# Performance work log

Hardware: AMD Instinct MI355X
Metric: run time of the kernel (lower is better)

Reference implementation:

```python
import jax, jax.numpy as jnp
import numpy as np

N, L, C = 4, 2048, 512
H, D = 8, 64          # head_num, head_channels; H*D == C so proj_in/out are Identity
FF = 4 * C            # GEGLU inner channels = 2048
EPS = 1e-5


def _layernorm(x, g, b):
    m = jnp.mean(x, axis=-1, keepdims=True)
    v = jnp.var(x, axis=-1, keepdims=True)
    return (x - m) * jax.lax.rsqrt(v + EPS) * g + b


def setup_inputs() -> dict:
    key = jax.random.key(0)
    ks = jax.random.split(key, 8)
    s = 0.02
    return {
        "x": jax.random.normal(ks[0], (N, L, C), dtype=jnp.float32),
        "ln0_g": jnp.ones((C,), jnp.float32),
        "ln0_b": jnp.zeros((C,), jnp.float32),
        "Wq": jax.random.normal(ks[1], (C, H * D), jnp.float32) * s,
        "bq": jnp.zeros((H * D,), jnp.float32),
        "Wk": jax.random.normal(ks[2], (C, H * D), jnp.float32) * s,
        "bk": jnp.zeros((H * D,), jnp.float32),
        "Wv": jax.random.normal(ks[3], (C, H * D), jnp.float32) * s,
        "bv": jnp.zeros((H * D,), jnp.float32),
        "ln1_g": jnp.ones((C,), jnp.float32),
        "ln1_b": jnp.zeros((C,), jnp.float32),
        "Wp": jax.random.normal(ks[4], (C, 2 * FF), jnp.float32) * s,
        "bp": jnp.zeros((2 * FF,), jnp.float32),
        "W2": jax.random.normal(ks[5], (FF, C), jnp.float32) * s,
        "b2": jnp.zeros((C,), jnp.float32),
    }


def reference(x, ln0_g, ln0_b, Wq, bq, Wk, bk, Wv, bv, ln1_g, ln1_b, Wp, bp, W2, b2):
    n, l, _ = x.shape
    # ---- self attention (CrossAttn with context = x) ----
    h = _layernorm(x, ln0_g, ln0_b)
    q = (h @ Wq + bq).reshape(n, l, H, D).transpose(0, 2, 1, 3)  # [n,H,l,D]
    k = (h @ Wk + bk).reshape(n, l, H, D).transpose(0, 2, 1, 3)
    v = (h @ Wv + bv).reshape(n, l, H, D).transpose(0, 2, 1, 3)
    scores = jnp.einsum('nhld,nhmd->nhlm', q, k) * (D ** -0.5)   # [n,H,l,l]
    attn = jax.nn.softmax(scores, axis=-1)
    o = jnp.einsum('nhlm,nhmd->nhld', attn, v)
    o = o.transpose(0, 2, 1, 3).reshape(n, l, H * D)
    # inner_channels == in_channels -> output projection is Identity (dropout=0)
    x = x + o
    # ---- feed forward: LayerNorm -> GEGLU -> Linear, residual ----
    h2 = _layernorm(x, ln1_g, ln1_b)
    pg = h2 @ Wp + bp                      # [n,l,2*FF]
    u, g = jnp.split(pg, 2, axis=-1)
    y = u * jax.nn.gelu(g, approximate=False)  # torch F.gelu default is exact erf
    return x + (y @ W2 + b2)
```

## Files before the change

### kernel.cpp

```cpp
#include <hip/hip_runtime.h>

typedef __attribute__((ext_vector_type(8))) short short8;
typedef __attribute__((ext_vector_type(4))) float f32x4;
typedef __attribute__((ext_vector_type(4))) unsigned short us4;

#define L_SEQ 2048
#define C_DIM 512
#define H_N 8
#define D_H 64
#define FF_DIM 2048

typedef __attribute__((address_space(3))) unsigned int as3_uint;
typedef const __attribute__((address_space(1))) unsigned int as1_uint;

__device__ __forceinline__ void gl16(const unsigned short* g, unsigned short* l) {
  __builtin_amdgcn_global_load_lds((as1_uint*)g, (as3_uint*)l, 16, 0, 0);
}

__device__ __forceinline__ unsigned short f2bf(float f) {
  unsigned int u = __float_as_uint(f);
  u = u + 0x7fffu + ((u >> 16) & 1u);
  return (unsigned short)(u >> 16);
}

__device__ __forceinline__ unsigned int cvtpk_bf16(float a, float b) {
  unsigned int r;
  asm("v_cvt_pk_bf16_f32 %0, %1, %2" : "=v"(r) : "v"(a), "v"(b));
  return r;
}

__global__ __launch_bounds__(256) void transpose_conv(
    const float* __restrict__ in, unsigned short* __restrict__ out,
    int R, int Ccols, int geglu) {
  __shared__ float tile[32][33];
  int tx = threadIdx.x & 31, ty = threadIdx.x >> 5;
  int c0 = blockIdx.x * 32, r0 = blockIdx.y * 32;
#pragma unroll
  for (int j = 0; j < 4; ++j) {
    int r = ty + j * 8;
    tile[r][tx] = in[(size_t)(r0 + r) * Ccols + c0 + tx];
  }
  __syncthreads();
#pragma unroll
  for (int j = 0; j < 4; ++j) {
    int rr = ty + j * 8;
    int n = c0 + rr;
    int J = n;
    if (geglu) {
      int hc = Ccols >> 1;
      J = (n < hc) ? (((n >> 4) << 5) + (n & 15))
                   : ((((n - hc) >> 4) << 5) + 16 + ((n - hc) & 15));
    }
    out[(size_t)J * R + r0 + tx] = f2bf(tile[tx][rr]);
  }
}

__global__ __launch_bounds__(256) void ln_kernel(
    const float* __restrict__ in, const float* __restrict__ g,
    const float* __restrict__ b, unsigned short* __restrict__ out) {
  int w = threadIdx.x >> 6, lane = threadIdx.x & 63;
  int row = blockIdx.x * 4 + w;
  const float4* p = (const float4*)(in + (size_t)row * C_DIM);
  float4 v0 = p[lane * 2], v1 = p[lane * 2 + 1];
  float s = v0.x + v0.y + v0.z + v0.w + v1.x + v1.y + v1.z + v1.w;
  float q = v0.x * v0.x + v0.y * v0.y + v0.z * v0.z + v0.w * v0.w +
            v1.x * v1.x + v1.y * v1.y + v1.z * v1.z + v1.w * v1.w;
#pragma unroll
  for (int m = 1; m < 64; m <<= 1) {
    s += __shfl_xor(s, m);
    q += __shfl_xor(q, m);
  }
  float mean = s * (1.0f / 512.0f);
  float var = q * (1.0f / 512.0f) - mean * mean;
  float rstd = rsqrtf(var + 1e-5f);
  const float4* gp = (const float4*)g;
  const float4* bp = (const float4*)b;
  float4 g0 = gp[lane * 2], g1 = gp[lane * 2 + 1];
  float4 b0 = bp[lane * 2], b1 = bp[lane * 2 + 1];
  short8 o;
  o[0] = (short)f2bf((v0.x - mean) * rstd * g0.x + b0.x);
  o[1] = (short)f2bf((v0.y - mean) * rstd * g0.y + b0.y);
  o[2] = (short)f2bf((v0.z - mean) * rstd * g0.z + b0.z);
  o[3] = (short)f2bf((v0.w - mean) * rstd * g0.w + b0.w);
  o[4] = (short)f2bf((v1.x - mean) * rstd * g1.x + b1.x);
  o[5] = (short)f2bf((v1.y - mean) * rstd * g1.y + b1.y);
  o[6] = (short)f2bf((v1.z - mean) * rstd * g1.z + b1.z);
  o[7] = (short)f2bf((v1.w - mean) * rstd * g1.w + b1.w);
  *((short8*)(out + (size_t)row * C_DIM) + lane) = o;
}

template <int EPI>
__global__ __launch_bounds__(256, 2) void gemm_kernel(
    const unsigned short* __restrict__ A, const unsigned short* __restrict__ Bt,
    int M, int N, int K,
    const float* __restrict__ bias0, const float* __restrict__ bias1,
    const float* __restrict__ bias2, const float* __restrict__ resid,
    void* __restrict__ outp) {
  __shared__ unsigned short As[128 * 32];
  __shared__ unsigned short Bs[128 * 32];
  int tid = threadIdx.x;
  int lane = tid & 63, w = tid >> 6;
  int wr = w >> 1, wc = w & 1;
  int hi = lane >> 4, l15 = lane & 15;
  int m0 = blockIdx.y * 128, n0 = blockIdx.x * 128;

  f32x4 acc[4][4];
#pragma unroll
  for (int i = 0; i < 4; ++i)
#pragma unroll
    for (int j = 0; j < 4; ++j) acc[i][j] = (f32x4){0.f, 0.f, 0.f, 0.f};

  int srow = w * 16 + (lane >> 2);
  int scol = (lane & 3) * 8;
  const unsigned short* aG0 = A + (size_t)(m0 + srow) * K + scol;
  const unsigned short* aG1 = A + (size_t)(m0 + 64 + srow) * K + scol;
  const unsigned short* bG0 = Bt + (size_t)(n0 + srow) * K + scol;
  const unsigned short* bG1 = Bt + (size_t)(n0 + 64 + srow) * K + scol;
  unsigned short* aL0 = &As[w * 512];
  unsigned short* aL1 = &As[2048 + w * 512];
  unsigned short* bL0 = &Bs[w * 512];
  unsigned short* bL1 = &Bs[2048 + w * 512];

  for (int k0 = 0; k0 < K; k0 += 32) {
    __syncthreads();
    gl16(aG0 + k0, aL0);
    gl16(aG1 + k0, aL1);
    gl16(bG0 + k0, bL0);
    gl16(bG1 + k0, bL1);
    __syncthreads();
    short8 af[4], bf[4];
#pragma unroll
    for (int mi = 0; mi < 4; ++mi)
      af[mi] = *(const short8*)&As[(wr * 64 + mi * 16 + l15) * 32 + hi * 8];
#pragma unroll
    for (int ni = 0; ni < 4; ++ni)
      bf[ni] = *(const short8*)&Bs[(wc * 64 + ni * 16 + l15) * 32 + hi * 8];
#pragma unroll
    for (int mi = 0; mi < 4; ++mi)
#pragma unroll
      for (int ni = 0; ni < 4; ++ni)
        acc[mi][ni] = __builtin_amdgcn_mfma_f32_16x16x32_bf16(
            af[mi], bf[ni], acc[mi][ni], 0, 0, 0);
  }

  if (EPI == 0) {
    unsigned short* out = (unsigned short*)outp;
#pragma unroll
    for (int mi = 0; mi < 4; ++mi) {
#pragma unroll
      for (int ni = 0; ni < 4; ++ni) {
        int col = n0 + wc * 64 + ni * 16 + l15;
        int t = col >> 9, jj = col & 511;
        int h = jj >> 6, d = jj & 63;
        const float* bptr = (t == 0) ? bias0 : (t == 1 ? bias1 : bias2);
        float bv = bptr[jj];
        int rbase = m0 + wr * 64 + mi * 16 + hi * 4;
        if (t == 2) {
          us4 pk;
#pragma unroll
          for (int i = 0; i < 4; ++i) pk[i] = f2bf(acc[mi][ni][i] + bv);
          int n = rbase >> 11, l = rbase & 2047;
          size_t dst = 8388608u + ((size_t)((n * H_N + h) * D_H + d)) * L_SEQ + l;
          *(us4*)(out + dst) = pk;
        } else {
#pragma unroll
          for (int i = 0; i < 4; ++i) {
            int m = rbase + i;
            int n = m >> 11, l = m & 2047;
            float val = acc[mi][ni][i] + bv;
            if (t == 0) val *= 0.18033688011112042f;
            size_t dst = (size_t)t * 4194304u +
                         (((size_t)(n * H_N + h)) * L_SEQ + l) * D_H + d;
            out[dst] = f2bf(val);
          }
        }
      }
    }
  } else if (EPI == 1) {
    unsigned short* out = (unsigned short*)outp;
#pragma unroll
    for (int mi = 0; mi < 4; ++mi) {
#pragma unroll
      for (int np = 0; np < 2; ++np) {
        int J16 = (n0 >> 4) + wc * 4 + np * 2;
        int ucol = (J16 >> 1) * 16 + l15;
        float bu = bias0[ucol], bg = bias0[2048 + ucol];
        int rbase = m0 + wr * 64 + mi * 16 + hi * 4;
#pragma unroll
        for (int i = 0; i < 4; ++i) {
          float uu = acc[mi][np * 2][i] + bu;
          float gg = acc[mi][np * 2 + 1][i] + bg;
          float ge = 0.5f * gg * (1.0f + erff(gg * 0.70710678118f));
          out[(size_t)(rbase + i) * FF_DIM + ucol] = f2bf(uu * ge);
        }
      }
    }
  } else {
    float* out = (float*)outp;
#pragma unroll
    for (int mi = 0; mi < 4; ++mi) {
#pragma unroll
      for (int ni = 0; ni < 4; ++ni) {
        int col = n0 + wc * 64 + ni * 16 + l15;
        float bv = bias0[col];
        int rbase = m0 + wr * 64 + mi * 16 + hi * 4;
#pragma unroll
        for (int i = 0; i < 4; ++i) {
          size_t idx = (size_t)(rbase + i) * C_DIM + col;
          out[idx] = acc[mi][ni][i] + bv + resid[idx];
        }
      }
    }
  }
}

__global__ __launch_bounds__(512, 6) void attn_kernel(
    const unsigned short* __restrict__ qkv, const float* __restrict__ x,
    float* __restrict__ x1) {
  __shared__ __align__(16) char lds_raw[43008];

  int tid = threadIdx.x, lane = tid & 63, w = tid >> 6;
  int half = w >> 2, wq = w & 3;
  int hi = lane >> 4, l15 = lane & 15;
  int bid = blockIdx.x;
  int k8 = bid & 7, j = bid >> 3;
  int nh = (k8 << 2) + (j & 3);
  int q0 = (j >> 2) << 6;
  int n = nh >> 3, h = nh & 7;
  const unsigned short* qb = qkv + (size_t)nh * (L_SEQ * D_H);
  const unsigned short* kb = qb + 4194304u;
  const unsigned short* vtb = qkv + 8388608u + (size_t)nh * (D_H * L_SEQ);

  short8 qf[2];
#pragma unroll
  for (int m = 0; m < 2; ++m)
    qf[m] = *(const short8*)(qb + (size_t)(q0 + wq * 16 + l15) * D_H + m * 32 + hi * 8);

  f32x4 O[4];
#pragma unroll
  for (int c = 0; c < 4; ++c) O[c] = (f32x4){0.f, 0.f, 0.f, 0.f};
  float lsum = 0.f;

  const int T0 = half << 10;
  int kr = wq * 8 + (lane >> 3);
  int kc = (((lane & 7) ^ (lane >> 3)) << 3);
  int vr = wq * 16 + (lane >> 2);
  int vc = (((lane & 3) ^ (vr & 3)) << 3);

#define KBb(bb) ((unsigned short*)(lds_raw + (((half << 1) | (bb)) << 12)))
#define VBb(bb) ((unsigned short*)(lds_raw + 16384 + (((half << 1) | (bb)) << 12)))
  unsigned int* plw = (unsigned int*)(lds_raw + 32768 + w * 1280);

#define STAGE(tt, bb)                                           \
  {                                                             \
    int t0s = T0 + (tt) * 32;                                   \
    gl16(kb + (size_t)(t0s + kr) * 64 + kc, KBb(bb) + wq * 512);\
    gl16(vtb + (size_t)vr * 2048 + t0s + vc, VBb(bb) + wq * 512);\
  }

  STAGE(0, 0)
  int buf = 0;
  int swz = (l15 & 7) << 4;

  for (int t = 0; t < 32; ++t) {
    __syncthreads();
    if (t < 31) STAGE(t + 1, buf ^ 1)

    const char* Kbase = (const char*)KBb(buf);
    short8 kf[2][2];
#pragma unroll
    for (int mc = 0; mc < 2; ++mc)
#pragma unroll
      for (int m = 0; m < 2; ++m) {
        int off = (mc * 16 + l15) * 128 + ((m * 64 + hi * 16) ^ swz);
        kf[mc][m] = *(const short8*)(Kbase + off);
      }

#pragma unroll
    for (int mc = 0; mc < 2; ++mc) {
      f32x4 s = (f32x4){0.f, 0.f, 0.f, 0.f};
      s = __builtin_amdgcn_mfma_f32_16x16x32_bf16(kf[mc][0], qf[0], s, 0, 0, 0);
      s = __builtin_amdgcn_mfma_f32_16x16x32_bf16(kf[mc][1], qf[1], s, 0, 0, 0);
      float p0 = __builtin_amdgcn_exp2f(s[0]);
      float p1 = __builtin_amdgcn_exp2f(s[1]);
      float p2 = __builtin_amdgcn_exp2f(s[2]);
      float p3 = __builtin_amdgcn_exp2f(s[3]);
      lsum += (p0 + p1) + (p2 + p3);
      uint2 pw;
      pw.x = cvtpk_bf16(p0, p1);
      pw.y = cvtpk_bf16(p2, p3);
      *(uint2*)((char*)plw + (l15 * 20 + mc * 8 + hi * 2) * 4) = pw;
    }

    short8 pf = *(const short8*)((const char*)plw + l15 * 80 + hi * 16);
    const char* Vbase = (const char*)VBb(buf);
#pragma unroll
    for (int c = 0; c < 4; ++c) {
      int off = (c * 16 + l15) * 64 + ((hi ^ (l15 & 3)) << 4);
      short8 vf = *(const short8*)(Vbase + off);
      O[c] = __builtin_amdgcn_mfma_f32_16x16x32_bf16(vf, pf, O[c], 0, 0, 0);
    }
    buf ^= 1;
  }

  __syncthreads();
  float* cm = (float*)lds_raw;
  float* my = cm + (size_t)(wq * 64 + lane) * 20;
  if (half == 1) {
#pragma unroll
    for (int c = 0; c < 4; ++c) *(f32x4*)(my + c * 4) = O[c];
    my[16] = lsum;
  }
  __syncthreads();
  if (half == 0) {
#pragma unroll
    for (int c = 0; c < 4; ++c) {
      f32x4 ob = *(const f32x4*)(my + c * 4);
      O[c][0] += ob[0]; O[c][1] += ob[1]; O[c][2] += ob[2]; O[c][3] += ob[3];
    }
    lsum += my[16];
    lsum += __shfl_xor(lsum, 16);
    lsum += __shfl_xor(lsum, 32);
    float invl = 1.0f / lsum;

    int tok = q0 + wq * 16 + l15;
    size_t base = ((size_t)(n * L_SEQ + tok)) * C_DIM + h * 64;
#pragma unroll
    for (int c = 0; c < 4; ++c) {
      const float4 xv = *(const float4*)(x + base + c * 16 + hi * 4);
      float4 ov;
      ov.x = xv.x + O[c][0] * invl;
      ov.y = xv.y + O[c][1] * invl;
      ov.z = xv.z + O[c][2] * invl;
      ov.w = xv.w + O[c][3] * invl;
      *(float4*)(x1 + base + c * 16 + hi * 4) = ov;
    }
  }
#undef STAGE
#undef KBb
#undef VBb
}

extern "C" void kernel_launch(void* const* d_in, const int* in_sizes, int n_in,
                              void* d_out, int out_size, void* d_ws,
                              size_t ws_size, hipStream_t stream) {
  const float* x = (const float*)d_in[0];
  const float* ln0g = (const float*)d_in[1];
  const float* ln0b = (const float*)d_in[2];
  const float* Wq = (const float*)d_in[3];
  const float* bq = (const float*)d_in[4];
  const float* Wk = (const float*)d_in[5];
  const float* bk = (const float*)d_in[6];
  const float* Wv = (const float*)d_in[7];
  const float* bv = (const float*)d_in[8];
  const float* ln1g = (const float*)d_in[9];
  const float* ln1b = (const float*)d_in[10];
  const float* Wp = (const float*)d_in[11];
  const float* bp = (const float*)d_in[12];
  const float* W2 = (const float*)d_in[13];
  const float* b2 = (const float*)d_in[14];

  char* ws = (char*)d_ws;
  unsigned short* hbuf = (unsigned short*)ws;
  unsigned short* qkvb = (unsigned short*)(ws + 8388608);
  unsigned short* ybuf = (unsigned short*)ws;
  float* x1 = (float*)(ws + 33554432);
  unsigned short* h2 = (unsigned short*)(ws + 33554432 + 16777216);
  unsigned short* wqkvt = (unsigned short*)(ws + 33554432 + 16777216 + 8388608);
  unsigned short* wpt = wqkvt + 1536 * 512;
  unsigned short* w2t = wpt + 4096 * 512;

  transpose_conv<<<dim3(16, 16), 256, 0, stream>>>(Wq, wqkvt, 512, 512, 0);
  transpose_conv<<<dim3(16, 16), 256, 0, stream>>>(Wk, wqkvt + 262144, 512, 512, 0);
  transpose_conv<<<dim3(16, 16), 256, 0, stream>>>(Wv, wqkvt + 524288, 512, 512, 0);
  transpose_conv<<<dim3(128, 16), 256, 0, stream>>>(Wp, wpt, 512, 4096, 1);
  transpose_conv<<<dim3(16, 64), 256, 0, stream>>>(W2, w2t, 2048, 512, 0);

  ln_kernel<<<2048, 256, 0, stream>>>(x, ln0g, ln0b, hbuf);
  gemm_kernel<0><<<dim3(12, 64), 256, 0, stream>>>(hbuf, wqkvt, 8192, 1536, 512,
                                                   bq, bk, bv, nullptr, qkvb);
  attn_kernel<<<1024, 512, 0, stream>>>(qkvb, x, x1);
  ln_kernel<<<2048, 256, 0, stream>>>(x1, ln1g, ln1b, h2);
  gemm_kernel<1><<<dim3(32, 64), 256, 0, stream>>>(h2, wpt, 8192, 4096, 512, bp,
                                                   nullptr, nullptr, nullptr, ybuf);
  gemm_kernel<2><<<dim3(4, 64), 256, 0, stream>>>(ybuf, w2t, 8192, 512, 2048, b2,
                                                  nullptr, nullptr, x1,
                                                  (float*)d_out);
}
```

Baseline: 280.4 us.

## Load attention V fragments directly from global and shrink final GEMM N-tile

The attention kernel stops staging transposed V tiles through LDS. Each wave now loads its V fragments straight from global memory into registers every iteration, which cuts LDS use from 43008 to 26624 bytes and could raise occupancy. The GEMM kernel is templated on N-tile width, and the last FFN projection (N=512) uses 64-wide tiles to launch twice as many blocks. The risks are uncoalesced, strided global V loads with no latency hiding in attention, and lower per-block reuse in the final GEMM.

```diff
diff --git a/kernel.cpp b/kernel.cpp
--- a/kernel.cpp
+++ b/kernel.cpp
@@ -89,26 +89,28 @@
   *((short8*)(out + (size_t)row * C_DIM) + lane) = o;
 }
 
-template <int EPI>
+template <int EPI, int TN>
 __global__ __launch_bounds__(256, 2) void gemm_kernel(
     const unsigned short* __restrict__ A, const unsigned short* __restrict__ Bt,
     int M, int N, int K,
     const float* __restrict__ bias0, const float* __restrict__ bias1,
     const float* __restrict__ bias2, const float* __restrict__ resid,
     void* __restrict__ outp) {
+  constexpr int NW = TN / 2;
+  constexpr int NF = TN / 32;
   __shared__ unsigned short As[128 * 32];
-  __shared__ unsigned short Bs[128 * 32];
+  __shared__ unsigned short Bs[TN * 32];
   int tid = threadIdx.x;
   int lane = tid & 63, w = tid >> 6;
   int wr = w >> 1, wc = w & 1;
   int hi = lane >> 4, l15 = lane & 15;
-  int m0 = blockIdx.y * 128, n0 = blockIdx.x * 128;
-
-  f32x4 acc[4][4];
+  int m0 = blockIdx.y * 128, n0 = blockIdx.x * TN;
+
+  f32x4 acc[4][NF];
 #pragma unroll
   for (int i = 0; i < 4; ++i)
 #pragma unroll
-    for (int j = 0; j < 4; ++j) acc[i][j] = (f32x4){0.f, 0.f, 0.f, 0.f};
+    for (int j = 0; j < NF; ++j) acc[i][j] = (f32x4){0.f, 0.f, 0.f, 0.f};
 
   int srow = w * 16 + (lane >> 2);
   int scol = (lane & 3) * 8;
@@ -126,19 +128,19 @@
     gl16(aG0 + k0, aL0);
     gl16(aG1 + k0, aL1);
     gl16(bG0 + k0, bL0);
-    gl16(bG1 + k0, bL1);
+    if (TN == 128) gl16(bG1 + k0, bL1);
     __syncthreads();
-    short8 af[4], bf[4];
+    short8 af[4], bf[NF];
 #pragma unroll
     for (int mi = 0; mi < 4; ++mi)
       af[mi] = *(const short8*)&As[(wr * 64 + mi * 16 + l15) * 32 + hi * 8];
 #pragma unroll
-    for (int ni = 0; ni < 4; ++ni)
-      bf[ni] = *(const short8*)&Bs[(wc * 64 + ni * 16 + l15) * 32 + hi * 8];
+    for (int ni = 0; ni < NF; ++ni)
+      bf[ni] = *(const short8*)&Bs[(wc * NW + ni * 16 + l15) * 32 + hi * 8];
 #pragma unroll
     for (int mi = 0; mi < 4; ++mi)
 #pragma unroll
-      for (int ni = 0; ni < 4; ++ni)
+      for (int ni = 0; ni < NF; ++ni)
         acc[mi][ni] = __builtin_amdgcn_mfma_f32_16x16x32_bf16(
             af[mi], bf[ni], acc[mi][ni], 0, 0, 0);
   }
@@ -148,8 +150,8 @@
 #pragma unroll
     for (int mi = 0; mi < 4; ++mi) {
 #pragma unroll
-      for (int ni = 0; ni < 4; ++ni) {
-        int col = n0 + wc * 64 + ni * 16 + l15;
+      for (int ni = 0; ni < NF; ++ni) {
+        int col = n0 + wc * NW + ni * 16 + l15;
         int t = col >> 9, jj = col & 511;
         int h = jj >> 6, d = jj & 63;
         const float* bptr = (t == 0) ? bias0 : (t == 1 ? bias1 : bias2);
@@ -200,8 +202,8 @@
 #pragma unroll
     for (int mi = 0; mi < 4; ++mi) {
 #pragma unroll
-      for (int ni = 0; ni < 4; ++ni) {
-        int col = n0 + wc * 64 + ni * 16 + l15;
+      for (int ni = 0; ni < NF; ++ni) {
+        int col = n0 + wc * NW + ni * 16 + l15;
         float bv = bias0[col];
         int rbase = m0 + wr * 64 + mi * 16 + hi * 4;
 #pragma unroll
@@ -217,7 +219,7 @@
 __global__ __launch_bounds__(512, 6) void attn_kernel(
     const unsigned short* __restrict__ qkv, const float* __restrict__ x,
     float* __restrict__ x1) {
-  __shared__ __align__(16) char lds_raw[43008];
+  __shared__ __align__(16) char lds_raw[26624];
 
   int tid = threadIdx.x, lane = tid & 63, w = tid >> 6;
   int half = w >> 2, wq = w & 3;
@@ -244,18 +246,14 @@
   const int T0 = half << 10;
   int kr = wq * 8 + (lane >> 3);
   int kc = (((lane & 7) ^ (lane >> 3)) << 3);
-  int vr = wq * 16 + (lane >> 2);
-  int vc = (((lane & 3) ^ (vr & 3)) << 3);
 
 #define KBb(bb) ((unsigned short*)(lds_raw + (((half << 1) | (bb)) << 12)))
-#define VBb(bb) ((unsigned short*)(lds_raw + 16384 + (((half << 1) | (bb)) << 12)))
-  unsigned int* plw = (unsigned int*)(lds_raw + 32768 + w * 1280);
-
-#define STAGE(tt, bb)                                           \
-  {                                                             \
-    int t0s = T0 + (tt) * 32;                                   \
-    gl16(kb + (size_t)(t0s + kr) * 64 + kc, KBb(bb) + wq * 512);\
-    gl16(vtb + (size_t)vr * 2048 + t0s + vc, VBb(bb) + wq * 512);\
+  unsigned int* plw = (unsigned int*)(lds_raw + 16384 + w * 1280);
+
+#define STAGE(tt, bb)                                            \
+  {                                                              \
+    int t0s = T0 + (tt) * 32;                                    \
+    gl16(kb + (size_t)(t0s + kr) * 64 + kc, KBb(bb) + wq * 512); \
   }
 
   STAGE(0, 0)
@@ -265,6 +263,12 @@
   for (int t = 0; t < 32; ++t) {
     __syncthreads();
     if (t < 31) STAGE(t + 1, buf ^ 1)
+
+    const unsigned short* vg = vtb + T0 + t * 32 + hi * 8;
+    short8 vf[4];
+#pragma unroll
+    for (int c = 0; c < 4; ++c)
+      vf[c] = *(const short8*)(vg + (size_t)(c * 16 + l15) * 2048);
 
     const char* Kbase = (const char*)KBb(buf);
     short8 kf[2][2];
@@ -293,13 +297,9 @@
     }
 
     short8 pf = *(const short8*)((const char*)plw + l15 * 80 + hi * 16);
-    const char* Vbase = (const char*)VBb(buf);
-#pragma unroll
-    for (int c = 0; c < 4; ++c) {
-      int off = (c * 16 + l15) * 64 + ((hi ^ (l15 & 3)) << 4);
-      short8 vf = *(const short8*)(Vbase + off);
-      O[c] = __builtin_amdgcn_mfma_f32_16x16x32_bf16(vf, pf, O[c], 0, 0, 0);
-    }
+#pragma unroll
+    for (int c = 0; c < 4; ++c)
+      O[c] = __builtin_amdgcn_mfma_f32_16x16x32_bf16(vf[c], pf, O[c], 0, 0, 0);
     buf ^= 1;
   }
 
@@ -338,7 +338,6 @@
   }
 #undef STAGE
 #undef KBb
-#undef VBb
 }
 
 extern "C" void kernel_launch(void* const* d_in, const int* in_sizes, int n_in,
@@ -377,13 +376,12 @@
   transpose_conv<<<dim3(16, 64), 256, 0, stream>>>(W2, w2t, 2048, 512, 0);
 
   ln_kernel<<<2048, 256, 0, stream>>>(x, ln0g, ln0b, hbuf);
-  gemm_kernel<0><<<dim3(12, 64), 256, 0, stream>>>(hbuf, wqkvt, 8192, 1536, 512,
-                                                   bq, bk, bv, nullptr, qkvb);
+  gemm_kernel<0, 128><<<dim3(12, 64), 256, 0, stream>>>(
+      hbuf, wqkvt, 8192, 1536, 512, bq, bk, bv, nullptr, qkvb);
   attn_kernel<<<1024, 512, 0, stream>>>(qkvb, x, x1);
   ln_kernel<<<2048, 256, 0, stream>>>(x1, ln1g, ln1b, h2);
-  gemm_kernel<1><<<dim3(32, 64), 256, 0, stream>>>(h2, wpt, 8192, 4096, 512, bp,
-                                                   nullptr, nullptr, nullptr, ybuf);
-  gemm_kernel<2><<<dim3(4, 64), 256, 0, stream>>>(ybuf, w2t, 8192, 512, 2048, b2,
-                                                  nullptr, nullptr, x1,
-                                                  (float*)d_out);
-}
+  gemm_kernel<1, 128><<<dim3(32, 64), 256, 0, stream>>>(
+      h2, wpt, 8192, 4096, 512, bp, nullptr, nullptr, nullptr, ybuf);
+  gemm_kernel<2, 64><<<dim3(8, 64), 256, 0, stream>>>(
+      ybuf, w2t, 8192, 512, 2048, b2, nullptr, nullptr, x1, (float*)d_out);
+}
```

After: 376.4 us. 1.34x slower.
